# Optimization experiments

Hardware: AMD Instinct MI355X
Metric: run time of the kernel (lower is better)

The kernel has to match this reference:

```python
import jax, jax.numpy as jnp
import numpy as np

N_NODES = 50000
N_EDGES = 800000
D = 64  # in_dim = hidden_dim = out_dim


def gcn_conv(x, edge_index, W, b, num_nodes):
    """PyG GCNConv: x' = D^{-1/2} (A + I) D^{-1/2} (x W) + b."""
    h = x @ W  # [N, out]
    # add self-loops
    loop = jnp.arange(num_nodes, dtype=edge_index.dtype)
    row = jnp.concatenate([edge_index[0], loop])  # sources j
    col = jnp.concatenate([edge_index[1], loop])  # targets i
    # symmetric normalization
    ones = jnp.ones(row.shape[0], dtype=h.dtype)
    deg = jax.ops.segment_sum(ones, col, num_segments=num_nodes)
    dinv = jnp.where(deg > 0, jax.lax.rsqrt(deg), 0.0)
    norm = dinv[row] * dinv[col]  # [E+N]
    # gather -> scale -> scatter-add
    msg = h[row] * norm[:, None]
    out = jax.ops.segment_sum(msg, col, num_segments=num_nodes)
    return out + b


def setup_inputs() -> dict:
    key = jax.random.key(0)
    k = jax.random.split(key, 6)
    x = jax.random.normal(k[0], (N_NODES, D), dtype=jnp.float32)
    edge_index = jax.random.randint(k[1], (2, N_EDGES), 0, N_NODES, dtype=jnp.int64)
    s = 1.0 / np.sqrt(D)
    W1 = jax.random.uniform(k[2], (D, D), jnp.float32, -s, s)
    b1 = jnp.zeros((D,), jnp.float32)
    W2 = jax.random.uniform(k[3], (D, D), jnp.float32, -s, s)
    b2 = jnp.zeros((D,), jnp.float32)
    return {"x": x, "edge_index": edge_index, "W1": W1, "b1": b1, "W2": W2, "b2": b2}


def reference(x, edge_index, W1, b1, W2, b2):
    h = gcn_conv(x, edge_index, W1, b1, N_NODES)
    h = jax.nn.relu(h)
    out = gcn_conv(h, edge_index, W2, b2, N_NODES)
    return out
```

## Files before the change

kernel.cpp:

```cpp
#include <hip/hip_runtime.h>
#include <hip/hip_fp16.h>

#define N_NODES 50000
#define N_EDGES 800000
#define D 64
#define RANGES 8
#define SLICES 16
#define NPB (N_NODES / RANGES)
#define I4S (N_EDGES / SLICES / 4)
#define CAPS 12
#define CAP  48

__global__ __launch_bounds__(1024)
void partition_kernel(const int* __restrict__ row, const int* __restrict__ col,
                      unsigned char* __restrict__ cnt8,
                      unsigned short* __restrict__ ebuf) {
    __shared__ int cur[NPB];
    int tid = threadIdx.x;
    int r   = blockIdx.x & (RANGES - 1);
    int s   = blockIdx.x / RANGES;
    int lo  = r * NPB;
    for (int i = tid; i < NPB; i += 1024) cur[i] = 0;
    __syncthreads();
    const int4* c4 = (const int4*)col;
    const int4* r4 = (const int4*)row;
    size_t ebase = (size_t)s * N_NODES * CAPS;
    for (int i = s * I4S + tid; i < (s + 1) * I4S; i += 1024) {
        int4 c  = c4[i];
        int4 rr = r4[i];
        int dx = c.x - lo, dy = c.y - lo, dz = c.z - lo, dw = c.w - lo;
        if ((unsigned)dx < NPB) {
            int p = atomicAdd(&cur[dx], 1);
            if (p < CAPS) ebuf[ebase + (size_t)(lo + dx) * CAPS + p] = (unsigned short)rr.x;
        }
        if ((unsigned)dy < NPB) {
            int p = atomicAdd(&cur[dy], 1);
            if (p < CAPS) ebuf[ebase + (size_t)(lo + dy) * CAPS + p] = (unsigned short)rr.y;
        }
        if ((unsigned)dz < NPB) {
            int p = atomicAdd(&cur[dz], 1);
            if (p < CAPS) ebuf[ebase + (size_t)(lo + dz) * CAPS + p] = (unsigned short)rr.z;
        }
        if ((unsigned)dw < NPB) {
            int p = atomicAdd(&cur[dw], 1);
            if (p < CAPS) ebuf[ebase + (size_t)(lo + dw) * CAPS + p] = (unsigned short)rr.w;
        }
    }
    __syncthreads();
    for (int i = tid; i < NPB; i += 1024)
        cnt8[(size_t)s * N_NODES + lo + i] = (unsigned char)min(cur[i], CAPS);
}

__global__ __launch_bounds__(256)
void compact_kernel(const unsigned char* __restrict__ cnt8,
                    const unsigned short* __restrict__ ebuf,
                    unsigned short* __restrict__ srcs,
                    float* __restrict__ dinv, int* __restrict__ cntf) {
    int tid = threadIdx.x, lane = tid & 63;
    int node = blockIdx.x * 4 + (tid >> 6);
    int c = 0;
    if (lane < SLICES) c = cnt8[(size_t)lane * N_NODES + node];
    int pin = c;
    #pragma unroll
    for (int off = 1; off < SLICES; off <<= 1) {
        int t = __shfl_up(pin, off, 64);
        if (lane >= off && lane < SLICES) pin += t;
    }
    int n = __shfl(pin, SLICES - 1, 64);
    int kk = 0, pp = 0;
    #pragma unroll
    for (int k = 0; k < SLICES; ++k) {
        int Pk = __shfl(pin, k, 64);
        if (lane >= Pk) { kk = k + 1; pp = Pk; }
    }
    unsigned short v = 0;
    if (lane < n && lane < CAP)
        v = ebuf[((size_t)kk * N_NODES + node) * CAPS + (lane - pp)];
    if (lane < CAP) srcs[(size_t)node * CAP + lane] = v;
    if (lane == 0) {
        cntf[node] = min(n, CAP);
        dinv[node] = rsqrtf((float)(n + 1));
    }
}

__global__ __launch_bounds__(256)
void gemm_kernel(const float* __restrict__ X, const float* __restrict__ W,
                 __half* __restrict__ H) {
    int tid = threadIdx.x, lane = tid & 63, wv = tid >> 6;
    float w[64];
    #pragma unroll
    for (int k = 0; k < 64; ++k) w[k] = W[k * 64 + lane];
    int node0 = blockIdx.x * 16 + wv * 4;
    #pragma unroll
    for (int r = 0; r < 4; ++r) {
        int node = node0 + r;
        float xv = X[node * 64 + lane];
        float a0 = 0.f, a1 = 0.f;
        #pragma unroll
        for (int k = 0; k < 64; k += 2) {
            a0 = fmaf(__shfl(xv, k, 64),     w[k],     a0);
            a1 = fmaf(__shfl(xv, k + 1, 64), w[k + 1], a1);
        }
        H[node * 64 + lane] = __float2half(a0 + a1);
    }
}

template<int FUSE>
__global__ __launch_bounds__(256)
void gather_kernel(const __half* __restrict__ H, const int* __restrict__ cnt,
                   const unsigned short* __restrict__ srcs,
                   const float* __restrict__ dinv,
                   const float* __restrict__ bias, const float* __restrict__ W2,
                   void* __restrict__ outp) {
    int tid = threadIdx.x, lane = tid & 63;
    int half = lane >> 5, sub = lane & 31;
    int node = blockIdx.x * 4 + (tid >> 6);
    int n = cnt[node];
    float di = dinv[node];
    const unsigned short* sp = srcs + (size_t)node * CAP;
    int e = 0;
    if (lane < n) {
        int s = sp[lane];
        float w = dinv[s];
        e = s | (((int)__half_as_ushort(__float2half(w))) << 16);
    }
    const __half2* H2 = (const __half2*)H;
    float2 self2 = __half22float2(H2[(size_t)node * 32 + sub]);
    float sw = (half == 0) ? di : 0.f;
    float ax = sw * self2.x, ay = sw * self2.y;
    int i0 = half;
    int nr = (n + 15) & ~15;
    for (int base = 0; base < nr; base += 16) {
        int b0 = base + i0;
        int q0 = __shfl(e, b0 + 0,  64), q1 = __shfl(e, b0 + 2,  64);
        int q2 = __shfl(e, b0 + 4,  64), q3 = __shfl(e, b0 + 6,  64);
        int q4 = __shfl(e, b0 + 8,  64), q5 = __shfl(e, b0 + 10, 64);
        int q6 = __shfl(e, b0 + 12, 64), q7 = __shfl(e, b0 + 14, 64);
        float2 v0 = __half22float2(H2[(size_t)(q0 & 0xFFFF) * 32 + sub]);
        float2 v1 = __half22float2(H2[(size_t)(q1 & 0xFFFF) * 32 + sub]);
        float2 v2 = __half22float2(H2[(size_t)(q2 & 0xFFFF) * 32 + sub]);
        float2 v3 = __half22float2(H2[(size_t)(q3 & 0xFFFF) * 32 + sub]);
        float2 v4 = __half22float2(H2[(size_t)(q4 & 0xFFFF) * 32 + sub]);
        float2 v5 = __half22float2(H2[(size_t)(q5 & 0xFFFF) * 32 + sub]);
        float2 v6 = __half22float2(H2[(size_t)(q6 & 0xFFFF) * 32 + sub]);
        float2 v7 = __half22float2(H2[(size_t)(q7 & 0xFFFF) * 32 + sub]);
        float w0 = __half2float(__ushort_as_half((unsigned short)((unsigned)q0 >> 16)));
        float w1 = __half2float(__ushort_as_half((unsigned short)((unsigned)q1 >> 16)));
        float w2 = __half2float(__ushort_as_half((unsigned short)((unsigned)q2 >> 16)));
        float w3 = __half2float(__ushort_as_half((unsigned short)((unsigned)q3 >> 16)));
        float w4 = __half2float(__ushort_as_half((unsigned short)((unsigned)q4 >> 16)));
        float w5 = __half2float(__ushort_as_half((unsigned short)((unsigned)q5 >> 16)));
        float w6 = __half2float(__ushort_as_half((unsigned short)((unsigned)q6 >> 16)));
        float w7 = __half2float(__ushort_as_half((unsigned short)((unsigned)q7 >> 16)));
        ax = fmaf(w0, v0.x, ax); ay = fmaf(w0, v0.y, ay);
        ax = fmaf(w1, v1.x, ax); ay = fmaf(w1, v1.y, ay);
        ax = fmaf(w2, v2.x, ax); ay = fmaf(w2, v2.y, ay);
        ax = fmaf(w3, v3.x, ax); ay = fmaf(w3, v3.y, ay);
        ax = fmaf(w4, v4.x, ax); ay = fmaf(w4, v4.y, ay);
        ax = fmaf(w5, v5.x, ax); ay = fmaf(w5, v5.y, ay);
        ax = fmaf(w6, v6.x, ax); ay = fmaf(w6, v6.y, ay);
        ax = fmaf(w7, v7.x, ax); ay = fmaf(w7, v7.y, ay);
    }
    ax += __shfl_xor(ax, 32, 64);
    ay += __shfl_xor(ay, 32, 64);
    float cx = __shfl(ax, lane >> 1, 64);
    float cy = __shfl(ay, lane >> 1, 64);
    float sum = (lane & 1) ? cy : cx;
    float gval = di * sum + bias[lane];
    if constexpr (FUSE) {
        gval = fmaxf(gval, 0.f);
        float wc[64];
        #pragma unroll
        for (int k = 0; k < 64; ++k) wc[k] = W2[k * 64 + lane];
        float o0 = 0.f, o1 = 0.f;
        #pragma unroll
        for (int k = 0; k < 64; k += 2) {
            o0 = fmaf(__shfl(gval, k, 64),     wc[k],     o0);
            o1 = fmaf(__shfl(gval, k + 1, 64), wc[k + 1], o1);
        }
        ((__half*)outp)[node * 64 + lane] = __float2half(o0 + o1);
    } else {
        ((float*)outp)[node * 64 + lane] = gval;
    }
}

extern "C" void kernel_launch(void* const* d_in, const int* in_sizes, int n_in,
                              void* d_out, int out_size, void* d_ws, size_t ws_size,
                              hipStream_t stream) {
    const float* x   = (const float*)d_in[0];
    const int*   ei  = (const int*)d_in[1];
    const int*   row = ei;
    const int*   col = ei + N_EDGES;
    const float* W1  = (const float*)d_in[2];
    const float* b1  = (const float*)d_in[3];
    const float* W2  = (const float*)d_in[4];
    const float* b2  = (const float*)d_in[5];
    float* out = (float*)d_out;

    char* p = (char*)d_ws;
    __half* h = (__half*)p;            p += (size_t)N_NODES * D * 2;
    char* A = p;                       p += 20000000;
    unsigned short* ebuf = (unsigned short*)A;
    unsigned char*  cnt8 = (unsigned char*)(A + 19200000);
    __half* h2 = (__half*)A;
    unsigned short* srcs = (unsigned short*)p; p += (size_t)N_NODES * CAP * 2;
    float* dinv = (float*)p;           p += (size_t)N_NODES * 4;
    int*   cntf = (int*)p;             p += (size_t)N_NODES * 4;

    partition_kernel<<<RANGES * SLICES, 1024, 0, stream>>>(row, col, cnt8, ebuf);
    compact_kernel<<<N_NODES / 4, 256, 0, stream>>>(cnt8, ebuf, srcs, dinv, cntf);
    gemm_kernel<<<N_NODES / 16, 256, 0, stream>>>(x, W1, h);
    gather_kernel<1><<<N_NODES / 4, 256, 0, stream>>>(h, cntf, srcs, dinv, b1, W2, h2);
    gather_kernel<0><<<N_NODES / 4, 256, 0, stream>>>(h2, cntf, srcs, dinv, b2, nullptr, out);
}
```

Measured before the change: 212.1 us.

## Make gather kernel persistent with software-pipelined neighbor prefetch and 8-byte row loads

The gather kernels become grid-stride persistent kernels (2048 blocks, one node per wave per iteration) that prefetch the next two nodes' counts, dinv and source lists, overlapping index and dinv loads with the current node's feature gathers. Each lane now loads 8 bytes (four halves) so a 64-wide row is covered by 16 lanes, and four neighbors are processed per wave step, with a two-stage xor reduction. W2 is read inside the loop instead of being cached in 64 registers, and launch bounds ask for 8 blocks per CU. Risks include fewer bytes in flight per neighbor step, repeated W2 loads per node, and extra shuffle reduction cost.

Result: slower. 291.2 us (+37.3%).

```diff
diff --git a/kernel.cpp b/kernel.cpp
--- a/kernel.cpp
+++ b/kernel.cpp
@@ -10,6 +10,8 @@
 #define I4S (N_EDGES / SLICES / 4)
 #define CAPS 12
 #define CAP  48
+#define GRID_G 2048
+#define NWAVES (GRID_G * 4)
 
 __global__ __launch_bounds__(1024)
 void partition_kernel(const int* __restrict__ row, const int* __restrict__ col,
@@ -105,82 +107,97 @@
     }
 }
 
+__device__ __forceinline__ void acc4(float w, float2 r,
+                                     float& a0, float& a1, float& a2, float& a3) {
+    __half2 h0 = __builtin_bit_cast(__half2, r.x);
+    __half2 h1 = __builtin_bit_cast(__half2, r.y);
+    float2 u = __half22float2(h0);
+    float2 v = __half22float2(h1);
+    a0 = fmaf(w, u.x, a0); a1 = fmaf(w, u.y, a1);
+    a2 = fmaf(w, v.x, a2); a3 = fmaf(w, v.y, a3);
+}
+
 template<int FUSE>
-__global__ __launch_bounds__(256)
+__global__ __launch_bounds__(256, 8)
 void gather_kernel(const __half* __restrict__ H, const int* __restrict__ cnt,
                    const unsigned short* __restrict__ srcs,
                    const float* __restrict__ dinv,
                    const float* __restrict__ bias, const float* __restrict__ W2,
                    void* __restrict__ outp) {
     int tid = threadIdx.x, lane = tid & 63;
-    int half = lane >> 5, sub = lane & 31;
-    int node = blockIdx.x * 4 + (tid >> 6);
-    int n = cnt[node];
-    float di = dinv[node];
-    const unsigned short* sp = srcs + (size_t)node * CAP;
-    int e = 0;
-    if (lane < n) {
-        int s = sp[lane];
-        float w = dinv[s];
-        e = s | (((int)__half_as_ushort(__float2half(w))) << 16);
-    }
-    const __half2* H2 = (const __half2*)H;
-    float2 self2 = __half22float2(H2[(size_t)node * 32 + sub]);
-    float sw = (half == 0) ? di : 0.f;
-    float ax = sw * self2.x, ay = sw * self2.y;
-    int i0 = half;
-    int nr = (n + 15) & ~15;
-    for (int base = 0; base < nr; base += 16) {
-        int b0 = base + i0;
-        int q0 = __shfl(e, b0 + 0,  64), q1 = __shfl(e, b0 + 2,  64);
-        int q2 = __shfl(e, b0 + 4,  64), q3 = __shfl(e, b0 + 6,  64);
-        int q4 = __shfl(e, b0 + 8,  64), q5 = __shfl(e, b0 + 10, 64);
-        int q6 = __shfl(e, b0 + 12, 64), q7 = __shfl(e, b0 + 14, 64);
-        float2 v0 = __half22float2(H2[(size_t)(q0 & 0xFFFF) * 32 + sub]);
-        float2 v1 = __half22float2(H2[(size_t)(q1 & 0xFFFF) * 32 + sub]);
-        float2 v2 = __half22float2(H2[(size_t)(q2 & 0xFFFF) * 32 + sub]);
-        float2 v3 = __half22float2(H2[(size_t)(q3 & 0xFFFF) * 32 + sub]);
-        float2 v4 = __half22float2(H2[(size_t)(q4 & 0xFFFF) * 32 + sub]);
-        float2 v5 = __half22float2(H2[(size_t)(q5 & 0xFFFF) * 32 + sub]);
-        float2 v6 = __half22float2(H2[(size_t)(q6 & 0xFFFF) * 32 + sub]);
-        float2 v7 = __half22float2(H2[(size_t)(q7 & 0xFFFF) * 32 + sub]);
-        float w0 = __half2float(__ushort_as_half((unsigned short)((unsigned)q0 >> 16)));
-        float w1 = __half2float(__ushort_as_half((unsigned short)((unsigned)q1 >> 16)));
-        float w2 = __half2float(__ushort_as_half((unsigned short)((unsigned)q2 >> 16)));
-        float w3 = __half2float(__ushort_as_half((unsigned short)((unsigned)q3 >> 16)));
-        float w4 = __half2float(__ushort_as_half((unsigned short)((unsigned)q4 >> 16)));
-        float w5 = __half2float(__ushort_as_half((unsigned short)((unsigned)q5 >> 16)));
-        float w6 = __half2float(__ushort_as_half((unsigned short)((unsigned)q6 >> 16)));
-        float w7 = __half2float(__ushort_as_half((unsigned short)((unsigned)q7 >> 16)));
-        ax = fmaf(w0, v0.x, ax); ay = fmaf(w0, v0.y, ay);
-        ax = fmaf(w1, v1.x, ax); ay = fmaf(w1, v1.y, ay);
-        ax = fmaf(w2, v2.x, ax); ay = fmaf(w2, v2.y, ay);
-        ax = fmaf(w3, v3.x, ax); ay = fmaf(w3, v3.y, ay);
-        ax = fmaf(w4, v4.x, ax); ay = fmaf(w4, v4.y, ay);
-        ax = fmaf(w5, v5.x, ax); ay = fmaf(w5, v5.y, ay);
-        ax = fmaf(w6, v6.x, ax); ay = fmaf(w6, v6.y, ay);
-        ax = fmaf(w7, v7.x, ax); ay = fmaf(w7, v7.y, ay);
-    }
-    ax += __shfl_xor(ax, 32, 64);
-    ay += __shfl_xor(ay, 32, 64);
-    float cx = __shfl(ax, lane >> 1, 64);
-    float cy = __shfl(ay, lane >> 1, 64);
-    float sum = (lane & 1) ? cy : cx;
-    float gval = di * sum + bias[lane];
-    if constexpr (FUSE) {
-        gval = fmaxf(gval, 0.f);
-        float wc[64];
-        #pragma unroll
-        for (int k = 0; k < 64; ++k) wc[k] = W2[k * 64 + lane];
-        float o0 = 0.f, o1 = 0.f;
-        #pragma unroll
-        for (int k = 0; k < 64; k += 2) {
-            o0 = fmaf(__shfl(gval, k, 64),     wc[k],     o0);
-            o1 = fmaf(__shfl(gval, k + 1, 64), wc[k + 1], o1);
-        }
-        ((__half*)outp)[node * 64 + lane] = __float2half(o0 + o1);
-    } else {
-        ((float*)outp)[node * 64 + lane] = gval;
+    int q = lane >> 4, sub = lane & 15;
+    int wid = (blockIdx.x << 2) + (tid >> 6);
+    const float2* Hf = (const float2*)H;
+
+    int node = wid;
+    int   nA  = cnt[node];
+    float diA = dinv[node];
+    int   sA  = (lane < CAP) ? (int)srcs[(size_t)node * CAP + lane] : 0;
+    int pn1 = min(node + NWAVES, N_NODES - 1);
+    int   nB  = cnt[pn1];
+    float diB = dinv[pn1];
+    int   sB  = (lane < CAP) ? (int)srcs[(size_t)pn1 * CAP + lane] : 0;
+    int eA = (lane < nA)
+           ? (sA | ((int)__half_as_ushort(__float2half(dinv[sA])) << 16)) : 0;
+
+    for (;;) {
+        int eB = (lane < nB)
+               ? (sB | ((int)__half_as_ushort(__float2half(dinv[sB])) << 16)) : 0;
+        int pn2 = min(node + 2 * NWAVES, N_NODES - 1);
+        int   nC  = cnt[pn2];
+        float diC = dinv[pn2];
+        int   sC  = (lane < CAP) ? (int)srcs[(size_t)pn2 * CAP + lane] : 0;
+
+        float2 sr = Hf[(size_t)node * 16 + sub];
+        float sw = (q == 0) ? diA : 0.f;
+        float a0 = 0.f, a1 = 0.f, a2 = 0.f, a3 = 0.f;
+        acc4(sw, sr, a0, a1, a2, a3);
+        int nr = (nA + 15) & ~15;
+        for (int base = 0; base < nr; base += 16) {
+            int e0 = __shfl(eA, base + q,      64);
+            int e1 = __shfl(eA, base + 4 + q,  64);
+            int e2 = __shfl(eA, base + 8 + q,  64);
+            int e3 = __shfl(eA, base + 12 + q, 64);
+            float2 r0 = Hf[(size_t)(e0 & 0xFFFF) * 16 + sub];
+            float2 r1 = Hf[(size_t)(e1 & 0xFFFF) * 16 + sub];
+            float2 r2 = Hf[(size_t)(e2 & 0xFFFF) * 16 + sub];
+            float2 r3 = Hf[(size_t)(e3 & 0xFFFF) * 16 + sub];
+            float w0 = __half2float(__ushort_as_half((unsigned short)((unsigned)e0 >> 16)));
+            float w1 = __half2float(__ushort_as_half((unsigned short)((unsigned)e1 >> 16)));
+            float w2 = __half2float(__ushort_as_half((unsigned short)((unsigned)e2 >> 16)));
+            float w3 = __half2float(__ushort_as_half((unsigned short)((unsigned)e3 >> 16)));
+            acc4(w0, r0, a0, a1, a2, a3);
+            acc4(w1, r1, a0, a1, a2, a3);
+            acc4(w2, r2, a0, a1, a2, a3);
+            acc4(w3, r3, a0, a1, a2, a3);
+        }
+        a0 += __shfl_xor(a0, 16, 64); a0 += __shfl_xor(a0, 32, 64);
+        a1 += __shfl_xor(a1, 16, 64); a1 += __shfl_xor(a1, 32, 64);
+        a2 += __shfl_xor(a2, 16, 64); a2 += __shfl_xor(a2, 32, 64);
+        a3 += __shfl_xor(a3, 16, 64); a3 += __shfl_xor(a3, 32, 64);
+        int sl = lane >> 2, jj = lane & 3;
+        float t0 = __shfl(a0, sl, 64), t1 = __shfl(a1, sl, 64);
+        float t2 = __shfl(a2, sl, 64), t3 = __shfl(a3, sl, 64);
+        float sum = (jj == 0) ? t0 : (jj == 1) ? t1 : (jj == 2) ? t2 : t3;
+        float gval = diA * sum + bias[lane];
+
+        if constexpr (FUSE) {
+            gval = fmaxf(gval, 0.f);
+            float o0 = 0.f, o1 = 0.f;
+            #pragma unroll
+            for (int k = 0; k < 64; k += 2) {
+                o0 = fmaf(__shfl(gval, k, 64),     W2[k * 64 + lane],       o0);
+                o1 = fmaf(__shfl(gval, k + 1, 64), W2[(k + 1) * 64 + lane], o1);
+            }
+            ((__half*)outp)[(size_t)node * 64 + lane] = __float2half(o0 + o1);
+        } else {
+            ((float*)outp)[(size_t)node * 64 + lane] = gval;
+        }
+
+        node += NWAVES;
+        if (node >= N_NODES) break;
+        nA = nB; diA = diB; eA = eB;
+        nB = nC; diB = diC; sB = sC;
     }
 }
 
@@ -210,6 +227,6 @@
     partition_kernel<<<RANGES * SLICES, 1024, 0, stream>>>(row, col, cnt8, ebuf);
     compact_kernel<<<N_NODES / 4, 256, 0, stream>>>(cnt8, ebuf, srcs, dinv, cntf);
     gemm_kernel<<<N_NODES / 16, 256, 0, stream>>>(x, W1, h);
-    gather_kernel<1><<<N_NODES / 4, 256, 0, stream>>>(h, cntf, srcs, dinv, b1, W2, h2);
-    gather_kernel<0><<<N_NODES / 4, 256, 0, stream>>>(h2, cntf, srcs, dinv, b2, nullptr, out);
-}
+    gather_kernel<1><<<GRID_G, 256, 0, stream>>>(h, cntf, srcs, dinv, b1, W2, h2);
+    gather_kernel<0><<<GRID_G, 256, 0, stream>>>(h2, cntf, srcs, dinv, b2, nullptr, out);
+}
```
